# Optimization experiments

Hardware: AMD Instinct MI355X
Metric: run time of the kernel (lower is better)

Reference implementation:

```python
import jax, jax.numpy as jnp
import numpy as np

N = 50000      # node_num
C = 64         # num_classes
G = 3          # number of metapath graphs (len(g))
E = 1200000    # edges per metapath graph
L = 2          # layers (PLPConv propagation steps)
D = 256        # input feature dim (feat_dims[0])
H = 256        # hidden_dim


def setup_inputs() -> dict:
    key = jax.random.key(0)
    ks = jax.random.split(key, 13)
    features0 = jax.random.normal(ks[0], (N, D), jnp.float32)
    labels = jax.random.randint(ks[1], (N,), 0, C)
    labels_one_hot = jax.nn.one_hot(labels, C, dtype=jnp.float32)
    # label_init: soft labels, rows on the simplex
    label_init = jax.nn.softmax(jax.random.normal(ks[2], (N, C), jnp.float32), axis=-1)
    train_mask = (jax.random.uniform(ks[3], (N, 1)) < 0.5).astype(jnp.float32)
    src = jax.random.randint(ks[4], (G, E), 0, N, dtype=jnp.int32)
    dst = jax.random.randint(ks[5], (G, E), 0, N, dtype=jnp.int32)
    # per-layer, per-graph learned edge logits (xavier-ish small init)
    e_edges = 0.1 * jax.random.normal(ks[6], (L, G, E), jnp.float32)
    attention = 0.5 * jax.random.normal(ks[7], (N, G), jnp.float32)
    alpha = 0.5 * jax.random.normal(ks[8], (N, 1), jnp.float32)
    W1 = jax.random.normal(ks[9], (D, H), jnp.float32) / np.sqrt(D)
    b1 = jnp.zeros((H,), jnp.float32)
    W2 = jax.random.normal(ks[10], (H, C), jnp.float32) / np.sqrt(H)
    b2 = jnp.zeros((C,), jnp.float32)
    return {"features0": features0, "label_init": label_init,
            "labels_one_hot": labels_one_hot, "train_mask": train_mask,
            "src": src, "dst": dst, "e_edges": e_edges,
            "attention": attention, "alpha": alpha,
            "W1": W1, "b1": b1, "W2": W2, "b2": b2}


def _edge_softmax(e, dst, n):
    # softmax of per-edge scalar over incoming edges of each dst node
    m = jax.ops.segment_max(e, dst, num_segments=n)
    a = jnp.exp(e - m[dst])
    s = jax.ops.segment_sum(a, dst, num_segments=n)
    return a / s[dst]


def reference(features0, label_init, labels_one_hot, train_mask,
              src, dst, e_edges, attention, alpha, W1, b1, W2, b2):
    n = label_init.shape[0]
    masked_label = 1.0 - train_mask            # (~masked).float(), [N,1]
    masked_oh = labels_one_hot * train_mask    # labels_one_hot * masked, [N,C]

    # Label propagation over each metapath graph (PLPConv stack, activation=None)
    h_prime = []
    for i in range(G):
        h = label_init
        for l in range(L):
            a = _edge_softmax(e_edges[l, i], dst[i], n)         # [E]
            msg = h[src[i]] * a[:, None]                        # gather-mul [E,C]
            h = jax.ops.segment_sum(msg, dst[i], num_segments=n)  # scatter-sum [N,C]
            h = h * masked_label + masked_oh                    # clamp train labels
        h_prime.append(h)
    x = jnp.stack(h_prime, axis=-1)                             # [N,C,G]

    att_mp = jax.nn.softmax(attention, axis=1)                  # [N,G]
    logits_lp = jnp.einsum('ncg,ng->nc', x, att_mp)             # [N,C]

    # MLP2 (2 layers, dropout=0): relu(x W1 + b1) W2 + b2
    hm = jax.nn.relu(features0 @ W1 + b1)
    logits_ns = hm @ W2 + b2                                    # [N,C]

    logits = jax.nn.sigmoid(alpha) * logits_lp + jax.nn.sigmoid(-alpha) * logits_ns
    return (logits, logits_lp, logits_ns)
```

## Files before the change

### kernel.cpp

```cpp
#include <hip/hip_runtime.h>
#include <hip/hip_bf16.h>

#define NN 50000
#define CC 64
#define GG 3
#define EE 1200000
#define LL 2
#define DD 256
#define HH 256
#define NB 196
#define NBK (GG * NB)
#define BKCAP 8192
#define CH 16384
#define CBLK 74


__device__ __forceinline__ ushort f2bf(float f) {
    unsigned b = __float_as_uint(f);
    return (ushort)((b + 0x7fffu + ((b >> 16) & 1u)) >> 16);
}
__device__ __forceinline__ float bf2f(unsigned u) {
    return __uint_as_float(u << 16);
}

typedef __attribute__((ext_vector_type(8))) short s8v;
typedef __attribute__((ext_vector_type(4))) float f4v;

template<int NWM, int NWN, bool A_FP32, bool OUT_RELU_BF16>
__global__ __launch_bounds__(256) void mfma_gemm_kernel(
    const void* __restrict__ Av, const ushort* __restrict__ Bt,
    const float* __restrict__ bias, void* __restrict__ Cv, int M, int Nc)
{
    static_assert(NWM * NWN == 4, "4 waves per block");
    const int tid = threadIdx.x;
    const int w = tid >> 6;
    const int l = tid & 63;
    const int wm = w / NWN;
    const int wn = w % NWN;
    const int r0 = blockIdx.x * (NWM * 64) + wm * 64;
    const int c0 = blockIdx.y * (NWN * 64) + wn * 64;
    const int lrow = l & 15;
    const int lk = (l >> 4) << 3;

    f4v acc[4][4] = {};

    for (int k0 = 0; k0 < 256; k0 += 32) {
        s8v a[4], b[4];
        #pragma unroll
        for (int i = 0; i < 4; i++) {
            int row = r0 + lrow + 16 * i;
            row = (row < M) ? row : (M - 1);
            if constexpr (A_FP32) {
                const float* Af = (const float*)Av;
                const float4* p = (const float4*)(Af + (size_t)row * 256 + k0 + lk);
                float4 f0 = p[0], f1 = p[1];
                union { ushort u[8]; s8v v; } t;
                t.u[0] = f2bf(f0.x); t.u[1] = f2bf(f0.y);
                t.u[2] = f2bf(f0.z); t.u[3] = f2bf(f0.w);
                t.u[4] = f2bf(f1.x); t.u[5] = f2bf(f1.y);
                t.u[6] = f2bf(f1.z); t.u[7] = f2bf(f1.w);
                a[i] = t.v;
            } else {
                const ushort* Ab = (const ushort*)Av;
                a[i] = *(const s8v*)(Ab + (size_t)row * 256 + k0 + lk);
            }
        }
        #pragma unroll
        for (int j = 0; j < 4; j++) {
            int col = c0 + lrow + 16 * j;
            b[j] = *(const s8v*)(Bt + (size_t)col * 256 + k0 + lk);
        }
        #pragma unroll
        for (int i = 0; i < 4; i++)
            #pragma unroll
            for (int j = 0; j < 4; j++)
                acc[i][j] = __builtin_amdgcn_mfma_f32_16x16x32_bf16(
                    a[i], b[j], acc[i][j], 0, 0, 0);
    }

    #pragma unroll
    for (int i = 0; i < 4; i++) {
        #pragma unroll
        for (int r = 0; r < 4; r++) {
            int row = r0 + 16 * i + (l >> 4) * 4 + r;
            if (row >= M) continue;
            #pragma unroll
            for (int j = 0; j < 4; j++) {
                int col = c0 + 16 * j + lrow;
                float v = acc[i][j][r] + bias[col];
                if constexpr (OUT_RELU_BF16) {
                    v = fmaxf(v, 0.f);
                    ((ushort*)Cv)[(size_t)row * Nc + col] = f2bf(v);
                } else {
                    ((float*)Cv)[(size_t)row * Nc + col] = v;
                }
            }
        }
    }
}

__global__ void wcvt_kernel(const float* __restrict__ W1,
                            const float* __restrict__ W2,
                            ushort* __restrict__ Wt1, ushort* __restrict__ Wt2)
{
    int idx = blockIdx.x * 256 + threadIdx.x;
    if (idx < 256 * 256) {
        int n = idx >> 8, k = idx & 255;
        Wt1[idx] = f2bf(W1[k * 256 + n]);
    } else {
        int i = idx - 256 * 256;
        if (i < 64 * 256) {
            int n = i >> 8, k = i & 255;
            Wt2[i] = f2bf(W2[k * 64 + n]);
        }
    }
}

__global__ __launch_bounds__(256) void prep_kernel(
    const float* __restrict__ label_init, const float* __restrict__ labels_oh,
    const float* __restrict__ train_mask, ushort* __restrict__ lab_bf,
    short* __restrict__ mid)
{
    int b = blockIdx.x;
    if (b < 3125) {
        int i = b * 256 + threadIdx.x;
        int v = i >> 4;
        int c4 = (i & 15) * 4;
        float4 f = ((const float4*)label_init)[i];
        ushort4 u;
        u.x = f2bf(f.x); u.y = f2bf(f.y); u.z = f2bf(f.z); u.w = f2bf(f.w);
        int pl = c4 >> 5;
        *(ushort4*)(lab_bf + (size_t)pl * NN * 32 + (size_t)v * 32 + (c4 & 31)) = u;
    } else {
        int t = threadIdx.x;
        int v = (b - 3125) * 16 + (t >> 4);
        int sl = t & 15;
        if (v < NN) {
            float4 f = ((const float4*)(labels_oh + (size_t)v * 64))[sl];
            float p = (float)(sl * 4);
            float s = f.x * p + f.y * (p + 1.f) + f.z * (p + 2.f) + f.w * (p + 3.f);
            s += __shfl_xor(s, 1); s += __shfl_xor(s, 2);
            s += __shfl_xor(s, 4); s += __shfl_xor(s, 8);
            if (sl == 0) {
                float tm = train_mask[v];
                mid[v] = (tm > 0.5f) ? (short)(s + 0.5f) : (short)-1;
            }
        }
    }
}

__global__ void scan_bucket(const int* __restrict__ fill, int* __restrict__ bs)
{
    __shared__ int sd[256];
    __shared__ int s_run;
    int t = threadIdx.x;
    if (t == 0) s_run = 0;
    __syncthreads();
    for (int base = 0; base < NBK; base += 256) {
        int i = base + t;
        int v = (i < NBK) ? fill[i] : 0;
        sd[t] = v;
        __syncthreads();
        for (int o = 1; o < 256; o <<= 1) {
            int x = (t >= o) ? sd[t - o] : 0;
            __syncthreads();
            sd[t] += x;
            __syncthreads();
        }
        int run = s_run;
        __syncthreads();
        if (i < NBK) bs[i] = run + sd[t] - v;
        if (t == 255) s_run = run + sd[255];
        __syncthreads();
    }
    if (t == 0) bs[NBK] = GG * EE;
}

__global__ __launch_bounds__(1024) void binA_kernel(
    const int* __restrict__ dst, const int* __restrict__ src,
    const float* __restrict__ e_edges, int* __restrict__ fill,
    uint2* __restrict__ staging)
{
    int blk = blockIdx.x;
    int g = blk / CBLK;
    int bi = blk - g * CBLK;
    int base = bi * CH;
    __shared__ uint2 rec[CH];
    __shared__ int cnt[NB];
    __shared__ int lstart[NB];
    __shared__ int cur[NB];
    __shared__ int gbase[NB];
    __shared__ int sd[256];
    int t = threadIdx.x;
    if (t < NB) cnt[t] = 0;
    __syncthreads();

    int myd[16];
    #pragma unroll
    for (int k = 0; k < 16; k++) {
        int e = base + k * 1024 + t;
        int d = (e < EE) ? dst[g * EE + e] : -1;
        myd[k] = d;
        if (d >= 0) atomicAdd(&cnt[d >> 8], 1);
    }
    __syncthreads();

    if (t < 256) sd[t] = (t < NB) ? cnt[t] : 0;
    __syncthreads();
    for (int o = 1; o < 256; o <<= 1) {
        int x = (t < 256 && t >= o) ? sd[t - o] : 0;
        __syncthreads();
        if (t < 256) sd[t] += x;
        __syncthreads();
    }
    if (t < NB) {
        int c = cnt[t];
        int ls = sd[t] - c;
        lstart[t] = ls;
        cur[t] = ls;
        int fo = (c > 0) ? atomicAdd(&fill[g * NB + t], c) : 0;
        gbase[t] = (g * NB + t) * BKCAP + fo;
    }
    __syncthreads();

    #pragma unroll
    for (int k = 0; k < 16; k++) {
        int d = myd[k];
        if (d >= 0) {
            int e = base + k * 1024 + t;
            int pos = atomicAdd(&cur[d >> 8], 1);
            int idxg = g * EE + e;
            uint2 r;
            r.x = ((unsigned)f2bf(e_edges[idxg]) << 16) |
                  (unsigned)f2bf(e_edges[(size_t)(GG + g) * EE + e]);
            r.y = ((unsigned)src[idxg] << 16) | (unsigned)(d & 255);
            rec[pos] = r;
        }
    }
    __syncthreads();

    int w = t >> 6, lane = t & 63;
    for (int b = w; b < NB; b += 16) {
        int c = cnt[b];
        int ls = lstart[b];
        uint2* dp = staging + (size_t)gbase[b];
        for (int i = lane; i < c; i += 64) dp[i] = rec[ls + i];
    }
}

__global__ __launch_bounds__(1024) void bucket_kernel(
    const uint2* __restrict__ staging, const int* __restrict__ fill,
    const int* __restrict__ out_start, int* __restrict__ row_start,
    unsigned* __restrict__ packed0, unsigned* __restrict__ packed1)
{
    int blk = blockIdx.x;
    int g = blk / NB;
    int bucket = blk - g * NB;
    int bn = bucket << 8;
    int bnodes = min(256, NN - bn);
    int n = fill[blk];
    int obase = out_start[blk];
    int segStart = obase - g * EE;
    const uint2* st = staging + (size_t)blk * BKCAP;

    __shared__ int hist[256];
    __shared__ int sd[256];
    __shared__ int cur[256];
    __shared__ float sm[512];
    __shared__ ushort ab0[BKCAP];
    __shared__ ushort ab1[BKCAP];
    __shared__ ushort sb[BKCAP];
    int t = threadIdx.x;
    if (t < 256) hist[t] = 0;
    if (t < 512) sm[t] = 0.f;
    __syncthreads();

    for (int i = t; i < n; i += 1024) {
        uint2 r = st[i];
        int dl = r.y & 0xff;
        atomicAdd(&hist[dl], 1);
        atomicAdd(&sm[dl], __expf(bf2f(r.x >> 16)));
        atomicAdd(&sm[256 + dl], __expf(bf2f(r.x & 0xffffu)));
    }
    __syncthreads();

    if (t < 256) sd[t] = hist[t];
    __syncthreads();
    for (int o = 1; o < 256; o <<= 1) {
        int x = (t < 256 && t >= o) ? sd[t - o] : 0;
        __syncthreads();
        if (t < 256) sd[t] += x;
        __syncthreads();
    }
    if (t < 256) {
        cur[t] = sd[t] - hist[t];
        if (t < bnodes)
            row_start[(size_t)g * (NN + 1) + bn + t] = segStart + sd[t] - hist[t];
        if (hist[t] > 0) {
            sm[t] = 1.f / sm[t];
            sm[256 + t] = 1.f / sm[256 + t];
        }
    }
    if (bucket == NB - 1 && t == 0) row_start[(size_t)g * (NN + 1) + NN] = EE;
    __syncthreads();

    for (int i = t; i < n; i += 1024) {
        uint2 r = st[i];
        int dl = r.y & 0xff;
        int pos = atomicAdd(&cur[dl], 1);
        ab0[pos] = f2bf(__expf(bf2f(r.x >> 16)) * sm[dl]);
        ab1[pos] = f2bf(__expf(bf2f(r.x & 0xffffu)) * sm[256 + dl]);
        sb[pos] = (ushort)(r.y >> 16);
    }
    __syncthreads();

    for (int i = t; i < n; i += 1024) {
        unsigned s = sb[i];
        packed0[(size_t)obase + i] = ((unsigned)ab0[i] << 16) | s;
        packed1[(size_t)obase + i] = ((unsigned)ab1[i] << 16) | s;
    }
}

__device__ __forceinline__ void tile_pass(unsigned packed, int cnt,
        const ushort* __restrict__ plane, unsigned loff, int sub, float acc[4])
{
    for (int q0 = 0; q0 < cnt; q0 += 32) {
        uint2 gv[4]; float w[4];
        #pragma unroll
        for (int u = 0; u < 4; u++) {
            unsigned pkq = __shfl(packed, q0 + 8 * u + sub);
            w[u] = __uint_as_float(pkq & 0xffff0000u);
            gv[u] = *(const uint2*)((const char*)plane +
                                    (((pkq & 0xffffu) << 6) | loff));
        }
        #pragma unroll
        for (int u = 0; u < 4; u++) {
            acc[0] = fmaf(__uint_as_float(gv[u].x << 16),          w[u], acc[0]);
            acc[1] = fmaf(__uint_as_float(gv[u].x & 0xffff0000u),  w[u], acc[1]);
            acc[2] = fmaf(__uint_as_float(gv[u].y << 16),          w[u], acc[2]);
            acc[3] = fmaf(__uint_as_float(gv[u].y & 0xffff0000u),  w[u], acc[3]);
        }
    }
}

__global__ __launch_bounds__(256) void prop0_kernel(
    const ushort* __restrict__ lab_bf, const short* __restrict__ mid,
    const int* __restrict__ row_start, const unsigned* __restrict__ packed0,
    ushort* __restrict__ h_buf)
{
    int blk = blockIdx.x;
    int x = blk & 7, q = blk >> 3;
    int pl = x & 1;
    int bIdx = q * 4 + (x >> 1);
    int w = threadIdx.x >> 6, lane = threadIdx.x & 63;
    int gv = bIdx * 4 + w;
    int g = gv / NN;
    int v = gv - g * NN;
    const int* rs = row_start + (size_t)g * (NN + 1);
    int s = rs[v], tE = rs[v + 1];
    const unsigned* pk = packed0 + (size_t)g * EE;
    const ushort* plane = lab_bf + (size_t)pl * NN * 32;

    unsigned loff = (lane & 7) << 3;
    int sub = lane >> 3;
    float a[4] = {};
    for (int base = s; base < tE; base += 64) {
        int j = base + lane;
        unsigned packed = (j < tE) ? __builtin_nontemporal_load(pk + j) : 0u;
        int cnt = min(64, tE - base);
        tile_pass(packed, cnt, plane, loff, sub, a);
    }
    #pragma unroll
    for (int c = 0; c < 4; c++) {
        a[c] += __shfl_xor(a[c], 8);
        a[c] += __shfl_xor(a[c], 16);
        a[c] += __shfl_xor(a[c], 32);
    }
    int m = mid[v];
    float ml = (m < 0) ? 1.f : 0.f;
    if (lane < 8) {
        int cb = lane * 4;
        int cg = pl * 32 + cb;
        ushort4 o;
        o.x = f2bf(a[0] * ml + ((cg + 0 == m) ? 1.f : 0.f));
        o.y = f2bf(a[1] * ml + ((cg + 1 == m) ? 1.f : 0.f));
        o.z = f2bf(a[2] * ml + ((cg + 2 == m) ? 1.f : 0.f));
        o.w = f2bf(a[3] * ml + ((cg + 3 == m) ? 1.f : 0.f));
        *(ushort4*)(h_buf + ((size_t)(g * 2 + pl)) * NN * 32 + (size_t)v * 32 + cb) = o;
    }
}

__global__ __launch_bounds__(256) void finalp_kernel(
    const ushort* __restrict__ h_buf, const float* __restrict__ attention,
    const int* __restrict__ row_start, const unsigned* __restrict__ packed1,
    float* __restrict__ partial)
{
    int blk = blockIdx.x;
    int x = blk & 7, q = blk >> 3;
    int combo, vblk;
    if (x < 2) {
        if (q >= 6250) return;
        combo = x; vblk = q;
    } else if (x < 6) {
        combo = x; vblk = q;
    } else {
        if (q >= 6250) return;
        combo = x - 6; vblk = 6250 + q;
    }
    int g = combo >> 1, pl = combo & 1;
    int w = threadIdx.x >> 6, lane = threadIdx.x & 63;
    int v = vblk * 4 + w;
    const int* rs = row_start + (size_t)g * (NN + 1);
    int s = rs[v], tE = rs[v + 1];
    const unsigned* pk = packed1 + (size_t)g * EE;
    const ushort* plane = h_buf + ((size_t)(g * 2 + pl)) * NN * 32;

    float t0 = attention[v * 3], t1 = attention[v * 3 + 1], t2 = attention[v * 3 + 2];
    float mxa = fmaxf(t0, fmaxf(t1, t2));
    float e0 = __expf(t0 - mxa), e1 = __expf(t1 - mxa), e2 = __expf(t2 - mxa);
    float ainv = 1.f / (e0 + e1 + e2);
    float aw = ((g == 0) ? e0 : (g == 1) ? e1 : e2) * ainv;

    unsigned loff = (lane & 7) << 3;
    int sub = lane >> 3;
    float a[4] = {};
    for (int base = s; base < tE; base += 64) {
        int j = base + lane;
        unsigned packed = (j < tE) ? __builtin_nontemporal_load(pk + j) : 0u;
        int cnt = min(64, tE - base);
        tile_pass(packed, cnt, plane, loff, sub, a);
    }
    #pragma unroll
    for (int c = 0; c < 4; c++) {
        a[c] += __shfl_xor(a[c], 8);
        a[c] += __shfl_xor(a[c], 16);
        a[c] += __shfl_xor(a[c], 32);
    }
    if (lane < 8) {
        float4 o;
        o.x = a[0] * aw; o.y = a[1] * aw; o.z = a[2] * aw; o.w = a[3] * aw;
        *(float4*)(partial + ((size_t)g * NN + v) * 64 + pl * 32 + lane * 4) = o;
    }
}

__global__ __launch_bounds__(256) void combine_kernel(
    const float* __restrict__ partial, const short* __restrict__ mid,
    const float* __restrict__ alpha, const float* __restrict__ out_ns,
    float* __restrict__ out_logits, float* __restrict__ out_lp)
{
    int i = blockIdx.x * 256 + threadIdx.x;
    int v = i >> 4;
    int c4 = (i & 15) * 4;
    size_t o = (size_t)v * 64 + c4;
    float4 p0 = *(const float4*)(partial + o);
    float4 p1 = *(const float4*)(partial + (size_t)NN * 64 + o);
    float4 p2 = *(const float4*)(partial + (size_t)2 * NN * 64 + o);
    int m = mid[v];
    float ml = (m < 0) ? 1.f : 0.f;
    float4 lp;
    lp.x = (p0.x + p1.x + p2.x) * ml + ((c4 + 0 == m) ? 1.f : 0.f);
    lp.y = (p0.y + p1.y + p2.y) * ml + ((c4 + 1 == m) ? 1.f : 0.f);
    lp.z = (p0.z + p1.z + p2.z) * ml + ((c4 + 2 == m) ? 1.f : 0.f);
    lp.w = (p0.w + p1.w + p2.w) * ml + ((c4 + 3 == m) ? 1.f : 0.f);
    *(float4*)(out_lp + o) = lp;
    float al = alpha[v];
    float sg = 1.f / (1.f + __expf(-al));
    float4 ns = *(const float4*)(out_ns + o);
    float4 lg;
    lg.x = sg * lp.x + (1.f - sg) * ns.x;
    lg.y = sg * lp.y + (1.f - sg) * ns.y;
    lg.z = sg * lp.z + (1.f - sg) * ns.z;
    lg.w = sg * lp.w + (1.f - sg) * ns.w;
    *(float4*)(out_logits + o) = lg;
}

extern "C" void kernel_launch(void* const* d_in, const int* in_sizes, int n_in,
                              void* d_out, int out_size, void* d_ws, size_t ws_size,
                              hipStream_t stream)
{
    const float* features0  = (const float*)d_in[0];
    const float* label_init = (const float*)d_in[1];
    const float* labels_oh  = (const float*)d_in[2];
    const float* train_mask = (const float*)d_in[3];
    const int*   src        = (const int*)d_in[4];
    const int*   dst        = (const int*)d_in[5];
    const float* e_edges    = (const float*)d_in[6];
    const float* attention  = (const float*)d_in[7];
    const float* alpha      = (const float*)d_in[8];
    const float* W1         = (const float*)d_in[9];
    const float* b1         = (const float*)d_in[10];
    const float* W2         = (const float*)d_in[11];
    const float* b2         = (const float*)d_in[12];

    float* out        = (float*)d_out;
    float* out_logits = out;
    float* out_lp     = out + (size_t)NN * CC;
    float* out_ns     = out + 2 * (size_t)NN * CC;

    char* base = (char*)d_ws;
    size_t off = 0;
    auto alloc = [&](size_t bytes) -> void* {
        void* p = base + off;
        off = (off + bytes + 255) & ~(size_t)255;
        return p;
    };
    int*      fill         = (int*)alloc((size_t)NBK * sizeof(int));
    size_t    zero_bytes   = off;
    int*      out_start    = (int*)alloc((size_t)(NBK + 1) * sizeof(int));
    int*      row_start    = (int*)alloc((size_t)GG * (NN + 1) * sizeof(int));
    uint2*    staging      = (uint2*)alloc((size_t)NBK * BKCAP * sizeof(uint2));
    unsigned* packed0      = (unsigned*)alloc((size_t)GG * EE * sizeof(unsigned));
    unsigned* packed1      = (unsigned*)alloc((size_t)GG * EE * sizeof(unsigned));
    ushort*   h_buf        = (ushort*)alloc((size_t)GG * NN * CC * sizeof(ushort));
    ushort*   lab_bf       = (ushort*)alloc((size_t)NN * CC * sizeof(ushort));
    short*    mid          = (short*)alloc((size_t)NN * sizeof(short));

    ushort* Wt1     = (ushort*)packed0;
    ushort* Wt2     = Wt1 + 256 * 256;
    ushort* hm_bf   = (ushort*)staging;
    float*  partial = (float*)staging;

    wcvt_kernel<<<(256 * 256 + 64 * 256) / 256, 256, 0, stream>>>(W1, W2, Wt1, Wt2);
    mfma_gemm_kernel<2, 2, true, true><<<dim3((NN + 127) / 128, 2), 256, 0, stream>>>(
        features0, Wt1, b1, hm_bf, NN, HH);
    mfma_gemm_kernel<4, 1, false, false><<<dim3((NN + 255) / 256, 1), 256, 0, stream>>>(
        hm_bf, Wt2, b2, out_ns, NN, CC);

    prep_kernel<<<6250, 256, 0, stream>>>(label_init, labels_oh, train_mask,
                                          lab_bf, mid);

    hipMemsetAsync(fill, 0, zero_bytes, stream);
    binA_kernel<<<GG * CBLK, 1024, 0, stream>>>(dst, src, e_edges, fill, staging);
    scan_bucket<<<1, 256, 0, stream>>>(fill, out_start);
    bucket_kernel<<<GG * NB, 1024, 0, stream>>>(
        staging, fill, out_start, row_start, packed0, packed1);

    prop0_kernel<<<9375 * 8, 256, 0, stream>>>(
        lab_bf, mid, row_start, packed0, h_buf);

    finalp_kernel<<<12500 * 8, 256, 0, stream>>>(
        h_buf, attention, row_start, packed1, partial);
    combine_kernel<<<3125, 256, 0, stream>>>(
        partial, mid, alpha, out_ns, out_logits, out_lp);
}
```

Measured before the change: 562.7 us.

## Stream CSR edges per 8-lane group with software prefetch in propagation kernels

The propagation kernels drop the one-wavefront-per-node layout with shuffle reductions. Each 8-lane group now walks the edge range of 8 consecutive nodes, prefetching gathers PD edges ahead, and flushes a node's result when it crosses a row boundary. This is meant to remove lane waste and reduction overhead, since nodes average about 24 edges against a 64-wide wavefront. Along the way, the bucket kernel writes packed edges directly instead of staging them in shared memory, the attention softmax is computed once in the prep kernel, and the weight conversion kernel is merged into prep. The cost is more uneven work across groups and a serial dependency on row boundaries.

Result: slower. 590.4 us (+4.9%).

```diff
diff --git a/kernel.cpp b/kernel.cpp
--- a/kernel.cpp
+++ b/kernel.cpp
@@ -13,6 +13,7 @@
 #define BKCAP 8192
 #define CH 16384
 #define CBLK 74
+#define PD 8
 
 
 __device__ __forceinline__ ushort f2bf(float f) {
@@ -99,31 +100,17 @@
     }
 }
 
-__global__ void wcvt_kernel(const float* __restrict__ W1,
-                            const float* __restrict__ W2,
-                            ushort* __restrict__ Wt1, ushort* __restrict__ Wt2)
-{
-    int idx = blockIdx.x * 256 + threadIdx.x;
-    if (idx < 256 * 256) {
-        int n = idx >> 8, k = idx & 255;
-        Wt1[idx] = f2bf(W1[k * 256 + n]);
-    } else {
-        int i = idx - 256 * 256;
-        if (i < 64 * 256) {
-            int n = i >> 8, k = i & 255;
-            Wt2[i] = f2bf(W2[k * 64 + n]);
-        }
-    }
-}
-
 __global__ __launch_bounds__(256) void prep_kernel(
     const float* __restrict__ label_init, const float* __restrict__ labels_oh,
-    const float* __restrict__ train_mask, ushort* __restrict__ lab_bf,
-    short* __restrict__ mid)
+    const float* __restrict__ train_mask, const float* __restrict__ attention,
+    const float* __restrict__ W1, const float* __restrict__ W2,
+    ushort* __restrict__ lab_bf, short* __restrict__ mid,
+    float* __restrict__ attw, ushort* __restrict__ Wt1, ushort* __restrict__ Wt2)
 {
     int b = blockIdx.x;
+    int t = threadIdx.x;
     if (b < 3125) {
-        int i = b * 256 + threadIdx.x;
+        int i = b * 256 + t;
         int v = i >> 4;
         int c4 = (i & 15) * 4;
         float4 f = ((const float4*)label_init)[i];
@@ -131,11 +118,21 @@
         u.x = f2bf(f.x); u.y = f2bf(f.y); u.z = f2bf(f.z); u.w = f2bf(f.w);
         int pl = c4 >> 5;
         *(ushort4*)(lab_bf + (size_t)pl * NN * 32 + (size_t)v * 32 + (c4 & 31)) = u;
-    } else {
-        int t = threadIdx.x;
+    } else if (b < 6250) {
         int v = (b - 3125) * 16 + (t >> 4);
         int sl = t & 15;
         if (v < NN) {
+            if (sl == 1) {
+                float t0 = attention[v * 3], t1 = attention[v * 3 + 1],
+                      t2 = attention[v * 3 + 2];
+                float mxa = fmaxf(t0, fmaxf(t1, t2));
+                float e0 = __expf(t0 - mxa), e1 = __expf(t1 - mxa),
+                      e2 = __expf(t2 - mxa);
+                float ai = 1.f / (e0 + e1 + e2);
+                attw[v * 3 + 0] = e0 * ai;
+                attw[v * 3 + 1] = e1 * ai;
+                attw[v * 3 + 2] = e2 * ai;
+            }
             float4 f = ((const float4*)(labels_oh + (size_t)v * 64))[sl];
             float p = (float)(sl * 4);
             float s = f.x * p + f.y * (p + 1.f) + f.z * (p + 2.f) + f.w * (p + 3.f);
@@ -145,6 +142,16 @@
                 float tm = train_mask[v];
                 mid[v] = (tm > 0.5f) ? (short)(s + 0.5f) : (short)-1;
             }
+        }
+    } else {
+        int idx = (b - 6250) * 256 + t;
+        if (idx < 256 * 256) {
+            int n = idx >> 8, k = idx & 255;
+            Wt1[idx] = f2bf(W1[k * 256 + n]);
+        } else {
+            int i = idx - 256 * 256;
+            int n = i >> 8, k = i & 255;
+            Wt2[i] = f2bf(W2[k * 64 + n]);
         }
     }
 }
@@ -267,9 +274,6 @@
     __shared__ int sd[256];
     __shared__ int cur[256];
     __shared__ float sm[512];
-    __shared__ ushort ab0[BKCAP];
-    __shared__ ushort ab1[BKCAP];
-    __shared__ ushort sb[BKCAP];
     int t = threadIdx.x;
     if (t < 256) hist[t] = 0;
     if (t < 512) sm[t] = 0.f;
@@ -308,42 +312,16 @@
         uint2 r = st[i];
         int dl = r.y & 0xff;
         int pos = atomicAdd(&cur[dl], 1);
-        ab0[pos] = f2bf(__expf(bf2f(r.x >> 16)) * sm[dl]);
-        ab1[pos] = f2bf(__expf(bf2f(r.x & 0xffffu)) * sm[256 + dl]);
-        sb[pos] = (ushort)(r.y >> 16);
-    }
-    __syncthreads();
-
-    for (int i = t; i < n; i += 1024) {
-        unsigned s = sb[i];
-        packed0[(size_t)obase + i] = ((unsigned)ab0[i] << 16) | s;
-        packed1[(size_t)obase + i] = ((unsigned)ab1[i] << 16) | s;
-    }
-}
-
-__device__ __forceinline__ void tile_pass(unsigned packed, int cnt,
-        const ushort* __restrict__ plane, unsigned loff, int sub, float acc[4])
-{
-    for (int q0 = 0; q0 < cnt; q0 += 32) {
-        uint2 gv[4]; float w[4];
-        #pragma unroll
-        for (int u = 0; u < 4; u++) {
-            unsigned pkq = __shfl(packed, q0 + 8 * u + sub);
-            w[u] = __uint_as_float(pkq & 0xffff0000u);
-            gv[u] = *(const uint2*)((const char*)plane +
-                                    (((pkq & 0xffffu) << 6) | loff));
-        }
-        #pragma unroll
-        for (int u = 0; u < 4; u++) {
-            acc[0] = fmaf(__uint_as_float(gv[u].x << 16),          w[u], acc[0]);
-            acc[1] = fmaf(__uint_as_float(gv[u].x & 0xffff0000u),  w[u], acc[1]);
-            acc[2] = fmaf(__uint_as_float(gv[u].y << 16),          w[u], acc[2]);
-            acc[3] = fmaf(__uint_as_float(gv[u].y & 0xffff0000u),  w[u], acc[3]);
-        }
-    }
-}
-
-__global__ __launch_bounds__(256) void prop0_kernel(
+        size_t o = (size_t)obase + pos;
+        unsigned srcv = r.y >> 16;
+        float a0 = __expf(bf2f(r.x >> 16)) * sm[dl];
+        float a1 = __expf(bf2f(r.x & 0xffffu)) * sm[256 + dl];
+        packed0[o] = ((unsigned)f2bf(a0) << 16) | srcv;
+        packed1[o] = ((unsigned)f2bf(a1) << 16) | srcv;
+    }
+}
+
+__global__ __launch_bounds__(256) void prop0_stream(
     const ushort* __restrict__ lab_bf, const short* __restrict__ mid,
     const int* __restrict__ row_start, const unsigned* __restrict__ packed0,
     ushort* __restrict__ h_buf)
@@ -351,96 +329,131 @@
     int blk = blockIdx.x;
     int x = blk & 7, q = blk >> 3;
     int pl = x & 1;
-    int bIdx = q * 4 + (x >> 1);
-    int w = threadIdx.x >> 6, lane = threadIdx.x & 63;
-    int gv = bIdx * 4 + w;
-    int g = gv / NN;
-    int v = gv - g * NN;
+    int u = q * 4 + (x >> 1);
+    int g = u / 196, vb = u - g * 196;
+    int tid = threadIdx.x;
+    int grp = tid >> 3, li = tid & 7;
+    int v0 = vb * 256 + grp * 8;
+    if (v0 >= NN) return;
+    int vend = min(v0 + 8, NN);
     const int* rs = row_start + (size_t)g * (NN + 1);
-    int s = rs[v], tE = rs[v + 1];
     const unsigned* pk = packed0 + (size_t)g * EE;
     const ushort* plane = lab_bf + (size_t)pl * NN * 32;
-
-    unsigned loff = (lane & 7) << 3;
-    int sub = lane >> 3;
-    float a[4] = {};
-    for (int base = s; base < tE; base += 64) {
-        int j = base + lane;
-        unsigned packed = (j < tE) ? __builtin_nontemporal_load(pk + j) : 0u;
-        int cnt = min(64, tE - base);
-        tile_pass(packed, cnt, plane, loff, sub, a);
-    }
-    #pragma unroll
-    for (int c = 0; c < 4; c++) {
-        a[c] += __shfl_xor(a[c], 8);
-        a[c] += __shfl_xor(a[c], 16);
-        a[c] += __shfl_xor(a[c], 32);
-    }
-    int m = mid[v];
-    float ml = (m < 0) ? 1.f : 0.f;
-    if (lane < 8) {
-        int cb = lane * 4;
-        int cg = pl * 32 + cb;
+    ushort* hout = h_buf + (size_t)(g * 2 + pl) * NN * 32;
+
+    int js = rs[v0], je = rs[vend];
+    int cv = v0;
+    int bound = rs[cv + 1];
+    float a0 = 0.f, a1 = 0.f, a2 = 0.f, a3 = 0.f;
+
+    auto flush = [&]() {
+        int m = mid[cv];
+        float ml = (m < 0) ? 1.f : 0.f;
+        int cb = pl * 32 + (li << 2);
         ushort4 o;
-        o.x = f2bf(a[0] * ml + ((cg + 0 == m) ? 1.f : 0.f));
-        o.y = f2bf(a[1] * ml + ((cg + 1 == m) ? 1.f : 0.f));
-        o.z = f2bf(a[2] * ml + ((cg + 2 == m) ? 1.f : 0.f));
-        o.w = f2bf(a[3] * ml + ((cg + 3 == m) ? 1.f : 0.f));
-        *(ushort4*)(h_buf + ((size_t)(g * 2 + pl)) * NN * 32 + (size_t)v * 32 + cb) = o;
-    }
-}
-
-__global__ __launch_bounds__(256) void finalp_kernel(
-    const ushort* __restrict__ h_buf, const float* __restrict__ attention,
+        o.x = f2bf(fmaf(a0, ml, (cb + 0 == m) ? 1.f : 0.f));
+        o.y = f2bf(fmaf(a1, ml, (cb + 1 == m) ? 1.f : 0.f));
+        o.z = f2bf(fmaf(a2, ml, (cb + 2 == m) ? 1.f : 0.f));
+        o.w = f2bf(fmaf(a3, ml, (cb + 3 == m) ? 1.f : 0.f));
+        *(ushort4*)(hout + (size_t)cv * 32 + (li << 2)) = o;
+        a0 = a1 = a2 = a3 = 0.f;
+    };
+    auto loadChunk = [&](int base, unsigned* w, uint2* r) {
+        #pragma unroll
+        for (int d = 0; d < PD; d++) {
+            int jj = base + d;
+            unsigned ww = (jj < je) ? pk[jj] : 0u;
+            w[d] = ww;
+            r[d] = *(const uint2*)(plane + ((ww & 0xffffu) << 5) + (li << 2));
+        }
+    };
+
+    unsigned wA[PD]; uint2 rA[PD];
+    loadChunk(js, wA, rA);
+    for (int jb = js; jb < je; jb += PD) {
+        unsigned wB[PD]; uint2 rB[PD];
+        loadChunk(jb + PD, wB, rB);
+        #pragma unroll
+        for (int d = 0; d < PD; d++) {
+            int j = jb + d;
+            if (j < je) {
+                while (j >= bound) { flush(); cv++; bound = rs[cv + 1]; }
+                float wt = __uint_as_float(wA[d] & 0xffff0000u);
+                a0 = fmaf(bf2f(rA[d].x & 0xffffu), wt, a0);
+                a1 = fmaf(bf2f(rA[d].x >> 16),     wt, a1);
+                a2 = fmaf(bf2f(rA[d].y & 0xffffu), wt, a2);
+                a3 = fmaf(bf2f(rA[d].y >> 16),     wt, a3);
+            }
+        }
+        #pragma unroll
+        for (int d = 0; d < PD; d++) { wA[d] = wB[d]; rA[d] = rB[d]; }
+    }
+    while (cv < vend) { flush(); cv++; }
+}
+
+__global__ __launch_bounds__(256) void finalp_stream(
+    const ushort* __restrict__ h_buf, const float* __restrict__ attw,
     const int* __restrict__ row_start, const unsigned* __restrict__ packed1,
     float* __restrict__ partial)
 {
     int blk = blockIdx.x;
     int x = blk & 7, q = blk >> 3;
-    int combo, vblk;
-    if (x < 2) {
-        if (q >= 6250) return;
-        combo = x; vblk = q;
-    } else if (x < 6) {
-        combo = x; vblk = q;
-    } else {
-        if (q >= 6250) return;
-        combo = x - 6; vblk = 6250 + q;
-    }
+    int combo, vb;
+    if (x < 6) { combo = x; vb = q; }
+    else       { combo = (x - 6) * 3 + q / 49; vb = 147 + q % 49; }
     int g = combo >> 1, pl = combo & 1;
-    int w = threadIdx.x >> 6, lane = threadIdx.x & 63;
-    int v = vblk * 4 + w;
+    int tid = threadIdx.x;
+    int grp = tid >> 3, li = tid & 7;
+    int v0 = vb * 256 + grp * 8;
+    if (v0 >= NN) return;
+    int vend = min(v0 + 8, NN);
     const int* rs = row_start + (size_t)g * (NN + 1);
-    int s = rs[v], tE = rs[v + 1];
     const unsigned* pk = packed1 + (size_t)g * EE;
-    const ushort* plane = h_buf + ((size_t)(g * 2 + pl)) * NN * 32;
-
-    float t0 = attention[v * 3], t1 = attention[v * 3 + 1], t2 = attention[v * 3 + 2];
-    float mxa = fmaxf(t0, fmaxf(t1, t2));
-    float e0 = __expf(t0 - mxa), e1 = __expf(t1 - mxa), e2 = __expf(t2 - mxa);
-    float ainv = 1.f / (e0 + e1 + e2);
-    float aw = ((g == 0) ? e0 : (g == 1) ? e1 : e2) * ainv;
-
-    unsigned loff = (lane & 7) << 3;
-    int sub = lane >> 3;
-    float a[4] = {};
-    for (int base = s; base < tE; base += 64) {
-        int j = base + lane;
-        unsigned packed = (j < tE) ? __builtin_nontemporal_load(pk + j) : 0u;
-        int cnt = min(64, tE - base);
-        tile_pass(packed, cnt, plane, loff, sub, a);
-    }
-    #pragma unroll
-    for (int c = 0; c < 4; c++) {
-        a[c] += __shfl_xor(a[c], 8);
-        a[c] += __shfl_xor(a[c], 16);
-        a[c] += __shfl_xor(a[c], 32);
-    }
-    if (lane < 8) {
+    const ushort* plane = h_buf + (size_t)(g * 2 + pl) * NN * 32;
+
+    int js = rs[v0], je = rs[vend];
+    int cv = v0;
+    int bound = rs[cv + 1];
+    float a0 = 0.f, a1 = 0.f, a2 = 0.f, a3 = 0.f;
+
+    auto flush = [&]() {
+        float aw = attw[cv * 3 + g];
         float4 o;
-        o.x = a[0] * aw; o.y = a[1] * aw; o.z = a[2] * aw; o.w = a[3] * aw;
-        *(float4*)(partial + ((size_t)g * NN + v) * 64 + pl * 32 + lane * 4) = o;
-    }
+        o.x = a0 * aw; o.y = a1 * aw; o.z = a2 * aw; o.w = a3 * aw;
+        *(float4*)(partial + ((size_t)g * NN + cv) * 64 + pl * 32 + (li << 2)) = o;
+        a0 = a1 = a2 = a3 = 0.f;
+    };
+    auto loadChunk = [&](int base, unsigned* w, uint2* r) {
+        #pragma unroll
+        for (int d = 0; d < PD; d++) {
+            int jj = base + d;
+            unsigned ww = (jj < je) ? pk[jj] : 0u;
+            w[d] = ww;
+            r[d] = *(const uint2*)(plane + ((ww & 0xffffu) << 5) + (li << 2));
+        }
+    };
+
+    unsigned wA[PD]; uint2 rA[PD];
+    loadChunk(js, wA, rA);
+    for (int jb = js; jb < je; jb += PD) {
+        unsigned wB[PD]; uint2 rB[PD];
+        loadChunk(jb + PD, wB, rB);
+        #pragma unroll
+        for (int d = 0; d < PD; d++) {
+            int j = jb + d;
+            if (j < je) {
+                while (j >= bound) { flush(); cv++; bound = rs[cv + 1]; }
+                float wt = __uint_as_float(wA[d] & 0xffff0000u);
+                a0 = fmaf(bf2f(rA[d].x & 0xffffu), wt, a0);
+                a1 = fmaf(bf2f(rA[d].x >> 16),     wt, a1);
+                a2 = fmaf(bf2f(rA[d].y & 0xffffu), wt, a2);
+                a3 = fmaf(bf2f(rA[d].y >> 16),     wt, a3);
+            }
+        }
+        #pragma unroll
+        for (int d = 0; d < PD; d++) { wA[d] = wB[d]; rA[d] = rB[d]; }
+    }
+    while (cv < vend) { flush(); cv++; }
 }
 
 __global__ __launch_bounds__(256) void combine_kernel(
@@ -514,32 +527,33 @@
     ushort*   h_buf        = (ushort*)alloc((size_t)GG * NN * CC * sizeof(ushort));
     ushort*   lab_bf       = (ushort*)alloc((size_t)NN * CC * sizeof(ushort));
     short*    mid          = (short*)alloc((size_t)NN * sizeof(short));
+    float*    attw         = (float*)alloc((size_t)NN * 3 * sizeof(float));
 
     ushort* Wt1     = (ushort*)packed0;
     ushort* Wt2     = Wt1 + 256 * 256;
     ushort* hm_bf   = (ushort*)staging;
     float*  partial = (float*)staging;
 
-    wcvt_kernel<<<(256 * 256 + 64 * 256) / 256, 256, 0, stream>>>(W1, W2, Wt1, Wt2);
+    hipMemsetAsync(fill, 0, zero_bytes, stream);
+    prep_kernel<<<6570, 256, 0, stream>>>(label_init, labels_oh, train_mask,
+                                          attention, W1, W2, lab_bf, mid, attw,
+                                          Wt1, Wt2);
+
     mfma_gemm_kernel<2, 2, true, true><<<dim3((NN + 127) / 128, 2), 256, 0, stream>>>(
         features0, Wt1, b1, hm_bf, NN, HH);
     mfma_gemm_kernel<4, 1, false, false><<<dim3((NN + 255) / 256, 1), 256, 0, stream>>>(
         hm_bf, Wt2, b2, out_ns, NN, CC);
 
-    prep_kernel<<<6250, 256, 0, stream>>>(label_init, labels_oh, train_mask,
-                                          lab_bf, mid);
-
-    hipMemsetAsync(fill, 0, zero_bytes, stream);
     binA_kernel<<<GG * CBLK, 1024, 0, stream>>>(dst, src, e_edges, fill, staging);
     scan_bucket<<<1, 256, 0, stream>>>(fill, out_start);
     bucket_kernel<<<GG * NB, 1024, 0, stream>>>(
         staging, fill, out_start, row_start, packed0, packed1);
 
-    prop0_kernel<<<9375 * 8, 256, 0, stream>>>(
+    prop0_stream<<<8 * 147, 256, 0, stream>>>(
         lab_bf, mid, row_start, packed0, h_buf);
 
-    finalp_kernel<<<12500 * 8, 256, 0, stream>>>(
-        h_buf, attention, row_start, packed1, partial);
+    finalp_stream<<<8 * 147, 256, 0, stream>>>(
+        h_buf, attw, row_start, packed1, partial);
     combine_kernel<<<3125, 256, 0, stream>>>(
         partial, mid, alpha, out_ns, out_logits, out_lp);
 }
```
